# Kernel optimization log

Measured on AMD Instinct MI355X. Metric: run time of the kernel, lower is better.

## Reference

```python
import jax, jax.numpy as jnp
import numpy as np

THRESHOLD = 0.5
NEG_POS_RATIO = 3
ALPHA = 1.0
N_CLASSES = 81
B, P, M = 32, 8732, 16


def cxcy_to_xy(c):
    return jnp.concatenate([c[..., :2] - c[..., 2:] / 2, c[..., :2] + c[..., 2:] / 2], -1)


def xy_to_cxcy(x):
    return jnp.concatenate([(x[..., :2] + x[..., 2:]) / 2, x[..., 2:] - x[..., :2]], -1)


def cxcy_to_gcxgcy(c, p):
    # SSD box encoding with variances 0.1 / 0.2
    return jnp.concatenate([(c[..., :2] - p[..., :2]) / (p[..., 2:] / 10.0),
                            jnp.log(c[..., 2:] / p[..., 2:]) * 5.0], -1)


def box_iou(a, b):
    # a: [M,4], b: [P,4] in xy (xmin,ymin,xmax,ymax)
    lt = jnp.maximum(a[:, None, :2], b[None, :, :2])
    rb = jnp.minimum(a[:, None, 2:], b[None, :, 2:])
    wh = jnp.clip(rb - lt, 0.0)
    inter = wh[..., 0] * wh[..., 1]
    area_a = (a[:, 2] - a[:, 0]) * (a[:, 3] - a[:, 1])
    area_b = (b[:, 2] - b[:, 0]) * (b[:, 3] - b[:, 1])
    return inter / (area_a[:, None] + area_b[None, :] - inter)


def setup_inputs() -> dict:
    key = jax.random.key(0)
    k1, k2, k3, k4, k5, k6, k7 = jax.random.split(key, 7)
    predicted_locs = jax.random.normal(k1, (B, P, 4), dtype=jnp.float32)
    predicted_logits = jax.random.normal(k2, (B, P, N_CLASSES), dtype=jnp.float32)
    # valid gt boxes: centers in (0.2,0.8), sizes in (0.05,0.4) -> xy
    cxy = jax.random.uniform(k3, (B, M, 2), minval=0.2, maxval=0.8)
    wh = jax.random.uniform(k4, (B, M, 2), minval=0.05, maxval=0.4)
    boxes = cxcy_to_xy(jnp.concatenate([cxy, wh], -1)).astype(jnp.float32)
    labels = jax.random.randint(k5, (B, M), 1, N_CLASSES)  # real objects: labels >= 1
    # priors: centers in (0,1), positive sizes
    pcxy = jax.random.uniform(k6, (P, 2), minval=0.0, maxval=1.0)
    pwh = jax.random.uniform(k7, (P, 2), minval=0.05, maxval=0.6)
    priors_cxcy = jnp.concatenate([pcxy, pwh], -1).astype(jnp.float32)
    return {"predicted_locs": predicted_locs, "predicted_logits": predicted_logits,
            "boxes": boxes, "labels": labels, "priors_cxcy": priors_cxcy}


def reference(predicted_locs, predicted_logits, boxes, labels, priors_cxcy):
    priors_xy = cxcy_to_xy(priors_cxcy)

    def match(bx, lb):  # bx: [M,4] xy, lb: [M] int
        overlap = box_iou(bx, priors_xy)                # [M, P]
        overlap_for_each_prior = overlap.max(axis=0)    # [P]
        object_for_each_prior = overlap.argmax(axis=0)  # [P]
        prior_for_each_object = overlap.argmax(axis=1)  # [M]
        # force each gt object to be matched to its best prior
        object_for_each_prior = object_for_each_prior.at[prior_for_each_object].set(jnp.arange(M))
        overlap_for_each_prior = overlap_for_each_prior.at[prior_for_each_object].set(1.0)
        label_for_each_prior = lb[object_for_each_prior]
        label_for_each_prior = jnp.where(overlap_for_each_prior < THRESHOLD, 0, label_for_each_prior)
        true_locs = cxcy_to_gcxgcy(xy_to_cxcy(bx[object_for_each_prior]), priors_cxcy)
        return true_locs, label_for_each_prior

    true_locs, true_classes = jax.vmap(match)(boxes, labels)  # [B,P,4], [B,P]

    positive = true_classes != 0                 # [B,P]
    n_positives = positive.sum(axis=1)           # [B]
    n_pos_total = n_positives.sum().astype(jnp.float32)

    # localization: L1Loss (mean) over positive priors only -> mean over 4*n_pos elements
    loc_loss = jnp.sum(jnp.abs(predicted_locs - true_locs) * positive[..., None]) / (4.0 * n_pos_total)

    # per-prior cross entropy, nan/inf -> 0 as in the original
    logp = jax.nn.log_softmax(predicted_logits, axis=-1)
    conf_loss_all = -jnp.take_along_axis(logp, true_classes[..., None], axis=-1)[..., 0]  # [B,P]
    conf_loss_all = jnp.nan_to_num(conf_loss_all, nan=0.0, posinf=0.0, neginf=0.0)

    conf_loss_pos_sum = jnp.sum(conf_loss_all * positive)
    conf_loss_neg = jnp.where(positive, 0.0, conf_loss_all)
    conf_loss_neg = -jnp.sort(-conf_loss_neg, axis=1)  # descending sort per image
    ranks = jnp.arange(P)[None, :]
    hard_negatives = ranks < (NEG_POS_RATIO * n_positives)[:, None]
    conf_loss_hard_neg_sum = jnp.sum(conf_loss_neg * hard_negatives)

    conf_loss = (conf_loss_hard_neg_sum + conf_loss_pos_sum) / n_pos_total
    return conf_loss + ALPHA * loc_loss
```

## Files before the change

kernel.cpp:

```cpp
#include <hip/hip_runtime.h>
#include <math.h>

#define BB 32
#define PP 8732
#define MM 16
#define NC 81
#define THRESH 0.5f
#define NPR 3
#define CHUNKS 16
#define CHUNK ((PP + CHUNKS - 1) / CHUNKS)
#define SBLK 64

__global__ void __launch_bounds__(256) match_part_kernel(
    const float* __restrict__ boxes,
    const float* __restrict__ priors,
    float* __restrict__ ovl,
    int* __restrict__ obj,
    unsigned long long* __restrict__ keys_part,
    unsigned* __restrict__ done)
{
    const int b = blockIdx.x / CHUNKS;
    const int c = blockIdx.x % CHUNKS;
    const int tid = threadIdx.x;
    if (blockIdx.x == 0 && tid == 0) *done = 0u;

    __shared__ float s_box[MM][4];
    __shared__ float s_area[MM];
    __shared__ float s_bv[4 * MM];
    __shared__ int   s_bi[4 * MM];

    if (tid < MM * 4) ((float*)s_box)[tid] = boxes[b * MM * 4 + tid];
    __syncthreads();
    if (tid < MM)
        s_area[tid] = (s_box[tid][2] - s_box[tid][0]) * (s_box[tid][3] - s_box[tid][1]);
    __syncthreads();

    float bestv[MM];
    int   bestp[MM];
#pragma unroll
    for (int m = 0; m < MM; ++m) { bestv[m] = -1.0f; bestp[m] = 0; }

    const int p0 = c * CHUNK;
    const int p1 = (p0 + CHUNK < PP) ? (p0 + CHUNK) : PP;
    for (int p = p0 + tid; p < p1; p += 256) {
        const float4 pr = ((const float4*)priors)[p];
        float px0 = pr.x - pr.z * 0.5f, py0 = pr.y - pr.w * 0.5f;
        float px1 = pr.x + pr.z * 0.5f, py1 = pr.y + pr.w * 0.5f;
        float parea = (px1 - px0) * (py1 - py0);
        float bv = -1.0f; int bm = 0;
#pragma unroll
        for (int m = 0; m < MM; ++m) {
            float lx = fmaxf(s_box[m][0], px0);
            float ly = fmaxf(s_box[m][1], py0);
            float rx = fminf(s_box[m][2], px1);
            float ry = fminf(s_box[m][3], py1);
            float w = fmaxf(rx - lx, 0.0f);
            float h = fmaxf(ry - ly, 0.0f);
            float inter = w * h;
            float iou = inter / (s_area[m] + parea - inter);
            if (iou > bv) { bv = iou; bm = m; }
            if (iou > bestv[m]) { bestv[m] = iou; bestp[m] = p; }
        }
        ovl[b * PP + p] = bv;
        obj[b * PP + p] = bm;
    }

    const int lane = tid & 63, wid = tid >> 6;
#pragma unroll
    for (int m = 0; m < MM; ++m) {
        float v = bestv[m]; int i = bestp[m];
        for (int off = 32; off > 0; off >>= 1) {
            float ov = __shfl_xor(v, off);
            int   oi = __shfl_xor(i, off);
            if (ov > v || (ov == v && oi < i)) { v = ov; i = oi; }
        }
        if (lane == 0) { s_bv[wid * MM + m] = v; s_bi[wid * MM + m] = i; }
    }
    __syncthreads();

    if (tid == 0) {
        for (int m = 0; m < MM; ++m) {
            float v = s_bv[m]; int i = s_bi[m];
            for (int w = 1; w < 4; ++w) {
                float ov = s_bv[w * MM + m]; int oi = s_bi[w * MM + m];
                if (ov > v || (ov == v && oi < i)) { v = ov; i = oi; }
            }
            if (v < 0.0f) v = 0.0f;
            keys_part[(b * CHUNKS + c) * MM + m] =
                ((unsigned long long)__float_as_uint(v) << 32) |
                (unsigned long long)(0x7FFFFFFFu - (unsigned)i);
        }
    }
}

__global__ void __launch_bounds__(256) conf_kernel(
    const float* __restrict__ logits,
    const float* __restrict__ plocs,
    const float* __restrict__ boxes,
    const int*   __restrict__ labels,
    const float* __restrict__ priors,
    const float* __restrict__ ovl,
    const int*   __restrict__ obj,
    const unsigned long long* __restrict__ keys_part,
    float* __restrict__ neg,
    int*   __restrict__ cnt_part,
    float* __restrict__ conf_part,
    float* __restrict__ loc_part)
{
    const int tid = threadIdx.x;
    const int lane = tid & 63;
    const int g = lane >> 4;
    const int i = lane & 15;
    const int b = blockIdx.x / SBLK;
    const int s = blockIdx.x % SBLK;

    __shared__ float s_box[MM][4];
    __shared__ int   s_lab[MM];
    __shared__ int   s_fp[MM];
    __shared__ unsigned long long s_keys[CHUNKS * MM];

    if (tid < MM * 4) ((float*)s_box)[tid] = boxes[b * MM * 4 + tid];
    if (tid < MM) s_lab[tid] = labels[b * MM + tid];
    s_keys[tid] = keys_part[b * CHUNKS * MM + tid];
    __syncthreads();
    if (tid < MM) {
        unsigned long long best = 0ull;
#pragma unroll
        for (int c = 0; c < CHUNKS; ++c) {
            unsigned long long k = s_keys[c * MM + tid];
            if (k > best) best = k;
        }
        s_fp[tid] = (int)(0x7FFFFFFFu - (unsigned)(best & 0xFFFFFFFFull));
    }
    __syncthreads();

    const int myfp = s_fp[i];

    const int w0 = s * 4 + (tid >> 6);
    const int GPI = PP / 4;

    int   pcnt = 0;
    float pconf = 0.0f, ploc = 0.0f;

    for (int wi = w0; wi < GPI; wi += SBLK * 4) {
        const int rp = wi * 4 + g;
        const int r = b * PP + rp;
        const float ov = ovl[r];
        const int om = obj[r];

        unsigned long long bal = __ballot(myfp == rp);
        unsigned gm = (unsigned)((bal >> (g * 16)) & 0xFFFFull);
        int o, cls;
        if (gm) { o = 31 - __clz(gm); cls = s_lab[o]; }
        else    { o = om; cls = (ov < THRESH) ? 0 : s_lab[om]; }

        const size_t base = (size_t)r * NC;
        float e0 = logits[base + i];
        float e1 = logits[base + 16 + i];
        float e2 = logits[base + 32 + i];
        float e3 = logits[base + 48 + i];
        float e4 = logits[base + 64 + i];
        float e5 = (i == 0) ? logits[base + 80] : -INFINITY;

        float mx = fmaxf(fmaxf(fmaxf(e0, e1), fmaxf(e2, e3)), fmaxf(e4, e5));
#pragma unroll
        for (int off = 8; off > 0; off >>= 1) mx = fmaxf(mx, __shfl_xor(mx, off));
        float sum = __expf(e0 - mx) + __expf(e1 - mx) + __expf(e2 - mx) +
                    __expf(e3 - mx) + __expf(e4 - mx) +
                    ((i == 0) ? __expf(e5 - mx) : 0.0f);
#pragma unroll
        for (int off = 8; off > 0; off >>= 1) sum += __shfl_xor(sum, off);

        const int k = cls >> 4, ci = cls & 15;
        float ek = (k == 0) ? e0 : (k == 1) ? e1 : (k == 2) ? e2 :
                   (k == 3) ? e3 : (k == 4) ? e4 : e5;
        float xc = __shfl(ek, (g << 4) + ci);
        float conf = mx + __logf(sum) - xc;
        if (!isfinite(conf)) conf = 0.0f;

        if (i == 0) {
            neg[r] = (cls == 0) ? conf : 0.0f;
            if (cls != 0) {
                pcnt += 1;
                pconf += conf;
                const float4 pr = ((const float4*)priors)[rp];
                float cx = (s_box[o][0] + s_box[o][2]) * 0.5f;
                float cy = (s_box[o][1] + s_box[o][3]) * 0.5f;
                float w4 = s_box[o][2] - s_box[o][0];
                float h4 = s_box[o][3] - s_box[o][1];
                float g0 = (cx - pr.x) / (pr.z / 10.0f);
                float g1 = (cy - pr.y) / (pr.w / 10.0f);
                float g2 = logf(w4 / pr.z) * 5.0f;
                float g3 = logf(h4 / pr.w) * 5.0f;
                const float4 pl = ((const float4*)plocs)[r];
                ploc += fabsf(pl.x - g0) + fabsf(pl.y - g1) +
                        fabsf(pl.z - g2) + fabsf(pl.w - g3);
            }
        }
    }

    __shared__ int   s4i[4];
    __shared__ float s4c[4], s4l[4];
#pragma unroll
    for (int off = 32; off > 0; off >>= 1) {
        pcnt  += __shfl_xor(pcnt, off);
        pconf += __shfl_xor(pconf, off);
        ploc  += __shfl_xor(ploc, off);
    }
    const int wv = tid >> 6;
    if (lane == 0) { s4i[wv] = pcnt; s4c[wv] = pconf; s4l[wv] = ploc; }
    __syncthreads();
    if (tid == 0) {
        cnt_part[blockIdx.x]  = s4i[0] + s4i[1] + s4i[2] + s4i[3];
        conf_part[blockIdx.x] = s4c[0] + s4c[1] + s4c[2] + s4c[3];
        loc_part[blockIdx.x]  = s4l[0] + s4l[1] + s4l[2] + s4l[3];
    }
}

#define TPK 1024
#define VPT ((PP + TPK - 1) / TPK)

__global__ void __launch_bounds__(TPK) topk_final_kernel(
    const float* __restrict__ neg, const int* __restrict__ cnt_part,
    const float* __restrict__ conf_part, const float* __restrict__ loc_part,
    float* __restrict__ hardneg, unsigned* __restrict__ done,
    float* __restrict__ out)
{
    const int b = blockIdx.x;
    const int tid = threadIdx.x;
    const int lane = tid & 63, wid = tid >> 6;
    __shared__ int s16a[16], s16b[16];
    __shared__ float s16f[16];
    __shared__ int s_k;
    __shared__ int s_last;

    if (tid < 64) {
        int c = cnt_part[b * SBLK + tid];
#pragma unroll
        for (int off = 32; off > 0; off >>= 1) c += __shfl_xor(c, off);
        if (tid == 0) s_k = NPR * c;
    }

    unsigned v[VPT];
#pragma unroll
    for (int j = 0; j < VPT; ++j) {
        int p = tid + j * TPK;
        v[j] = (p < PP) ? __float_as_uint(neg[b * PP + p]) : 0u;
    }
    __syncthreads();

    int K = s_k;
    if (K > PP) K = PP;
    if (K > 0) {
        unsigned lo = 0u;
        {
            const unsigned m1 = 0x40000000u;
            int c1 = 0;
#pragma unroll
            for (int j = 0; j < VPT; ++j) c1 += (v[j] >= m1);
#pragma unroll
            for (int off = 32; off > 0; off >>= 1) c1 += __shfl_xor(c1, off);
            if (lane == 0) s16a[wid] = c1;
            __syncthreads();
            int n1 = 0;
#pragma unroll
            for (int j = 0; j < 16; ++j) n1 += s16a[j];
            __syncthreads();
            if (n1 >= K) lo = m1;
        }
        unsigned span = 0x40000000u;
        for (int it = 0; it < 15; ++it) {
            span >>= 2;
            const unsigned m1 = lo + span;
            const unsigned m2 = lo + 2 * span;
            const unsigned m3 = lo + 3 * span;
            int c12 = 0, c3 = 0;
#pragma unroll
            for (int j = 0; j < VPT; ++j) {
                c12 += (v[j] >= m1) + ((int)(v[j] >= m2) << 16);
                c3  += (v[j] >= m3);
            }
#pragma unroll
            for (int off = 32; off > 0; off >>= 1) {
                c12 += __shfl_xor(c12, off);
                c3  += __shfl_xor(c3, off);
            }
            if (lane == 0) { s16a[wid] = c12; s16b[wid] = c3; }
            __syncthreads();
            int t12 = 0, t3 = 0;
#pragma unroll
            for (int j = 0; j < 16; ++j) { t12 += s16a[j]; t3 += s16b[j]; }
            __syncthreads();
            const int n1 = t12 & 0xFFFF, n2 = t12 >> 16, n3 = t3;
            lo = (n3 >= K) ? m3 : (n2 >= K) ? m2 : (n1 >= K) ? m1 : lo;
        }
        const unsigned kth = lo;

        int cgt = 0; float sgt = 0.0f;
#pragma unroll
        for (int j = 0; j < VPT; ++j) {
            if (v[j] > kth) { cgt++; sgt += __uint_as_float(v[j]); }
        }
#pragma unroll
        for (int off = 32; off > 0; off >>= 1) {
            cgt += __shfl_xor(cgt, off);
            sgt += __shfl_xor(sgt, off);
        }
        if (lane == 0) { s16a[wid] = cgt; s16f[wid] = sgt; }
        __syncthreads();
        if (tid == 0) {
            int cgt_t = 0; float sum_gt = 0.0f;
#pragma unroll
            for (int j = 0; j < 16; ++j) { cgt_t += s16a[j]; sum_gt += s16f[j]; }
            hardneg[b] = sum_gt + (float)(K - cgt_t) * __uint_as_float(kth);
        }
    } else {
        if (tid == 0) hardneg[b] = 0.0f;
    }

    __threadfence();
    if (tid == 0) {
        unsigned old = atomicAdd(done, 1u);
        s_last = (old == BB - 1) ? 1 : 0;
    }
    __syncthreads();
    if (!s_last) return;
    __threadfence();

    int np = 0; float cf = 0.0f, lc = 0.0f, hn = 0.0f;
    for (int j = tid; j < BB * SBLK; j += TPK) {
        np += cnt_part[j];
        cf += conf_part[j];
        lc += loc_part[j];
    }
    if (tid < BB) hn = hardneg[tid];
#pragma unroll
    for (int off = 32; off > 0; off >>= 1) {
        np += __shfl_xor(np, off);
        cf += __shfl_xor(cf, off);
        lc += __shfl_xor(lc, off);
        hn += __shfl_xor(hn, off);
    }
    __shared__ float s16l[16], s16h[16];
    if (lane == 0) { s16a[wid] = np; s16f[wid] = cf; s16l[wid] = lc; s16h[wid] = hn; }
    __syncthreads();
    if (tid == 0) {
        int npt_i = 0; float cft = 0.0f, lct = 0.0f, hnt = 0.0f;
#pragma unroll
        for (int j = 0; j < 16; ++j) {
            npt_i += s16a[j]; cft += s16f[j]; lct += s16l[j]; hnt += s16h[j];
        }
        float npt = (float)npt_i;
        out[0] = (hnt + cft) / npt + lct / (4.0f * npt);
    }
}

extern "C" void kernel_launch(void* const* d_in, const int* in_sizes, int n_in,
                              void* d_out, int out_size, void* d_ws, size_t ws_size,
                              hipStream_t stream) {
    (void)in_sizes; (void)n_in; (void)out_size; (void)ws_size;
    const float* plocs  = (const float*)d_in[0];
    const float* logits = (const float*)d_in[1];
    const float* boxes  = (const float*)d_in[2];
    const int*   labels = (const int*)d_in[3];
    const float* priors = (const float*)d_in[4];
    float* out = (float*)d_out;

    char* ws = (char*)d_ws;
    float* ovl      = (float*)ws; ws += (size_t)BB * PP * 4;
    int*   obj      = (int*)ws;   ws += (size_t)BB * PP * 4;
    float* neg      = (float*)ws; ws += (size_t)BB * PP * 4;
    unsigned long long* keys_part = (unsigned long long*)ws; ws += (size_t)BB * CHUNKS * MM * 8;
    int*   cnt_part  = (int*)ws;   ws += BB * SBLK * 4;
    float* conf_part = (float*)ws; ws += BB * SBLK * 4;
    float* loc_part  = (float*)ws; ws += BB * SBLK * 4;
    float* hardneg   = (float*)ws; ws += BB * 4;
    unsigned* done   = (unsigned*)ws; ws += 4;


    match_part_kernel<<<BB * CHUNKS, 256, 0, stream>>>(boxes, priors, ovl, obj,
                                                       keys_part, done);

    conf_kernel<<<BB * SBLK, 256, 0, stream>>>(logits, plocs, boxes, labels, priors,
                                               ovl, obj, keys_part, neg,
                                               cnt_part, conf_part, loc_part);

    topk_final_kernel<<<BB, TPK, 0, stream>>>(neg, cnt_part, conf_part, loc_part,
                                              hardneg, done, out);
}
```

Measured before the change: 81.15 us.

## Pack overlap and object index, move forced matching to a separate kernel

The match kernel now writes the per-prior best IoU and best object index as one 64-bit word instead of two separate arrays. A new single-block kernel reduces the per-chunk best-prior keys and overwrites the packed entries of the forced-match priors with IoU 1.0. This takes the ballot-based forced-match check and the per-block key reduction out of the conf kernel. The conf kernel also loads the first 64 logits per prior as one float4 per lane rather than four strided scalars, and picks the target logit by component and lane. In exchange there is an extra serialized launch, and the float4 loads are not 16-byte aligned because each row holds 81 floats.

```diff
diff --git a/kernel.cpp b/kernel.cpp
--- a/kernel.cpp
+++ b/kernel.cpp
@@ -14,8 +14,7 @@
 __global__ void __launch_bounds__(256) match_part_kernel(
     const float* __restrict__ boxes,
     const float* __restrict__ priors,
-    float* __restrict__ ovl,
-    int* __restrict__ obj,
+    unsigned long long* __restrict__ packed,
     unsigned long long* __restrict__ keys_part,
     unsigned* __restrict__ done)
 {
@@ -61,8 +60,9 @@
             if (iou > bv) { bv = iou; bm = m; }
             if (iou > bestv[m]) { bestv[m] = iou; bestp[m] = p; }
         }
-        ovl[b * PP + p] = bv;
-        obj[b * PP + p] = bm;
+        packed[b * PP + p] =
+            ((unsigned long long)__float_as_uint(bv < 0.0f ? 0.0f : bv) << 32) |
+            (unsigned long long)(unsigned)bm;
     }
 
     const int lane = tid & 63, wid = tid >> 6;
@@ -93,15 +93,39 @@
     }
 }
 
+__global__ void __launch_bounds__(512) force_match_kernel(
+    const unsigned long long* __restrict__ keys_part,
+    unsigned long long* __restrict__ packed)
+{
+    __shared__ int s_p[BB * MM];
+    const int tid = threadIdx.x;
+    const int b = tid >> 4, m = tid & 15;
+
+    unsigned long long best = 0ull;
+#pragma unroll
+    for (int c = 0; c < CHUNKS; ++c) {
+        unsigned long long k = keys_part[(b * CHUNKS + c) * MM + m];
+        if (k > best) best = k;
+    }
+    s_p[tid] = (int)(0x7FFFFFFFu - (unsigned)(best & 0xFFFFFFFFull));
+    __syncthreads();
+
+    if (m == 0) {
+        const unsigned long long one = (unsigned long long)__float_as_uint(1.0f) << 32;
+        for (int mm = 0; mm < MM; ++mm) {
+            int p = s_p[(b << 4) + mm];
+            packed[b * PP + p] = one | (unsigned long long)(unsigned)mm;
+        }
+    }
+}
+
 __global__ void __launch_bounds__(256) conf_kernel(
     const float* __restrict__ logits,
     const float* __restrict__ plocs,
     const float* __restrict__ boxes,
     const int*   __restrict__ labels,
     const float* __restrict__ priors,
-    const float* __restrict__ ovl,
-    const int*   __restrict__ obj,
-    const unsigned long long* __restrict__ keys_part,
+    const unsigned long long* __restrict__ packed,
     float* __restrict__ neg,
     int*   __restrict__ cnt_part,
     float* __restrict__ conf_part,
@@ -116,25 +140,10 @@
 
     __shared__ float s_box[MM][4];
     __shared__ int   s_lab[MM];
-    __shared__ int   s_fp[MM];
-    __shared__ unsigned long long s_keys[CHUNKS * MM];
 
     if (tid < MM * 4) ((float*)s_box)[tid] = boxes[b * MM * 4 + tid];
     if (tid < MM) s_lab[tid] = labels[b * MM + tid];
-    s_keys[tid] = keys_part[b * CHUNKS * MM + tid];
-    __syncthreads();
-    if (tid < MM) {
-        unsigned long long best = 0ull;
-#pragma unroll
-        for (int c = 0; c < CHUNKS; ++c) {
-            unsigned long long k = s_keys[c * MM + tid];
-            if (k > best) best = k;
-        }
-        s_fp[tid] = (int)(0x7FFFFFFFu - (unsigned)(best & 0xFFFFFFFFull));
-    }
-    __syncthreads();
-
-    const int myfp = s_fp[i];
+    __syncthreads();
 
     const int w0 = s * 4 + (tid >> 6);
     const int GPI = PP / 4;
@@ -145,36 +154,35 @@
     for (int wi = w0; wi < GPI; wi += SBLK * 4) {
         const int rp = wi * 4 + g;
         const int r = b * PP + rp;
-        const float ov = ovl[r];
-        const int om = obj[r];
-
-        unsigned long long bal = __ballot(myfp == rp);
-        unsigned gm = (unsigned)((bal >> (g * 16)) & 0xFFFFull);
-        int o, cls;
-        if (gm) { o = 31 - __clz(gm); cls = s_lab[o]; }
-        else    { o = om; cls = (ov < THRESH) ? 0 : s_lab[om]; }
+        const unsigned long long pk = packed[r];
+        const float ov = __uint_as_float((unsigned)(pk >> 32));
+        const int om = (int)(pk & 0xFFFFull);
+        const int cls = (ov < THRESH) ? 0 : s_lab[om];
 
         const size_t base = (size_t)r * NC;
-        float e0 = logits[base + i];
-        float e1 = logits[base + 16 + i];
-        float e2 = logits[base + 32 + i];
-        float e3 = logits[base + 48 + i];
+        const float4 f = *(const float4*)(logits + base + 4 * i);
         float e4 = logits[base + 64 + i];
         float e5 = (i == 0) ? logits[base + 80] : -INFINITY;
 
-        float mx = fmaxf(fmaxf(fmaxf(e0, e1), fmaxf(e2, e3)), fmaxf(e4, e5));
+        float mx = fmaxf(fmaxf(fmaxf(f.x, f.y), fmaxf(f.z, f.w)), fmaxf(e4, e5));
 #pragma unroll
         for (int off = 8; off > 0; off >>= 1) mx = fmaxf(mx, __shfl_xor(mx, off));
-        float sum = __expf(e0 - mx) + __expf(e1 - mx) + __expf(e2 - mx) +
-                    __expf(e3 - mx) + __expf(e4 - mx) +
+        float sum = __expf(f.x - mx) + __expf(f.y - mx) + __expf(f.z - mx) +
+                    __expf(f.w - mx) + __expf(e4 - mx) +
                     ((i == 0) ? __expf(e5 - mx) : 0.0f);
 #pragma unroll
         for (int off = 8; off > 0; off >>= 1) sum += __shfl_xor(sum, off);
 
-        const int k = cls >> 4, ci = cls & 15;
-        float ek = (k == 0) ? e0 : (k == 1) ? e1 : (k == 2) ? e2 :
-                   (k == 3) ? e3 : (k == 4) ? e4 : e5;
-        float xc = __shfl(ek, (g << 4) + ci);
+        float xc;
+        if (cls < 64) {
+            const int comp = cls & 3;
+            float cand = comp == 0 ? f.x : comp == 1 ? f.y : comp == 2 ? f.z : f.w;
+            xc = __shfl(cand, (g << 4) + (cls >> 2));
+        } else if (cls < 80) {
+            xc = __shfl(e4, (g << 4) + (cls - 64));
+        } else {
+            xc = __shfl(e5, (g << 4));
+        }
         float conf = mx + __logf(sum) - xc;
         if (!isfinite(conf)) conf = 0.0f;
 
@@ -183,6 +191,7 @@
             if (cls != 0) {
                 pcnt += 1;
                 pconf += conf;
+                const int o = om;
                 const float4 pr = ((const float4*)priors)[rp];
                 float cx = (s_box[o][0] + s_box[o][2]) * 0.5f;
                 float cy = (s_box[o][1] + s_box[o][3]) * 0.5f;
@@ -367,10 +376,9 @@
     float* out = (float*)d_out;
 
     char* ws = (char*)d_ws;
-    float* ovl      = (float*)ws; ws += (size_t)BB * PP * 4;
-    int*   obj      = (int*)ws;   ws += (size_t)BB * PP * 4;
-    float* neg      = (float*)ws; ws += (size_t)BB * PP * 4;
+    unsigned long long* packed    = (unsigned long long*)ws; ws += (size_t)BB * PP * 8;
     unsigned long long* keys_part = (unsigned long long*)ws; ws += (size_t)BB * CHUNKS * MM * 8;
+    float* neg       = (float*)ws; ws += (size_t)BB * PP * 4;
     int*   cnt_part  = (int*)ws;   ws += BB * SBLK * 4;
     float* conf_part = (float*)ws; ws += BB * SBLK * 4;
     float* loc_part  = (float*)ws; ws += BB * SBLK * 4;
@@ -378,11 +386,13 @@
     unsigned* done   = (unsigned*)ws; ws += 4;
 
 
-    match_part_kernel<<<BB * CHUNKS, 256, 0, stream>>>(boxes, priors, ovl, obj,
+    match_part_kernel<<<BB * CHUNKS, 256, 0, stream>>>(boxes, priors, packed,
                                                        keys_part, done);
 
+    force_match_kernel<<<1, 512, 0, stream>>>(keys_part, packed);
+
     conf_kernel<<<BB * SBLK, 256, 0, stream>>>(logits, plocs, boxes, labels, priors,
-                                               ovl, obj, keys_part, neg,
+                                               packed, neg,
                                                cnt_part, conf_part, loc_part);
 
     topk_final_kernel<<<BB, TPK, 0, stream>>>(neg, cnt_part, conf_part, loc_part,
```

Result: no change. 82.60 us (+1.8%).

## Apply forced prior matches in a separate tiny kernel instead of per-iteration ballot

Applied to the files above, without the earlier changes.

Moves the forced best-prior-per-object assignment out of the conf kernel into a new single-block kernel that writes obj and ovl=1.0 directly for each object's best prior. The conf kernel then drops its shared-memory key reduction, two barriers and per-iteration ballot, reading labels and boxes straight from global memory. This trades per-block setup and per-row ballot work for an extra kernel launch and a serialized dependency between stages.

```diff
diff --git a/kernel.cpp b/kernel.cpp
--- a/kernel.cpp
+++ b/kernel.cpp
@@ -93,6 +93,32 @@
     }
 }
 
+__global__ void __launch_bounds__(512) force_match_kernel(
+    const unsigned long long* __restrict__ keys_part,
+    float* __restrict__ ovl, int* __restrict__ obj)
+{
+    __shared__ int s_p[BB * MM];
+    const int tid = threadIdx.x;
+    const int b = tid >> 4, m = tid & 15;
+
+    unsigned long long best = 0ull;
+#pragma unroll
+    for (int c = 0; c < CHUNKS; ++c) {
+        unsigned long long k = keys_part[(b * CHUNKS + c) * MM + m];
+        if (k > best) best = k;
+    }
+    s_p[tid] = (int)(0x7FFFFFFFu - (unsigned)(best & 0xFFFFFFFFull));
+    __syncthreads();
+
+    if (m == 0) {
+        for (int mm = 0; mm < MM; ++mm) {
+            int p = s_p[(b << 4) + mm];
+            obj[b * PP + p] = mm;
+            ovl[b * PP + p] = 1.0f;
+        }
+    }
+}
+
 __global__ void __launch_bounds__(256) conf_kernel(
     const float* __restrict__ logits,
     const float* __restrict__ plocs,
@@ -101,7 +127,6 @@
     const float* __restrict__ priors,
     const float* __restrict__ ovl,
     const int*   __restrict__ obj,
-    const unsigned long long* __restrict__ keys_part,
     float* __restrict__ neg,
     int*   __restrict__ cnt_part,
     float* __restrict__ conf_part,
@@ -113,29 +138,6 @@
     const int i = lane & 15;
     const int b = blockIdx.x / SBLK;
     const int s = blockIdx.x % SBLK;
-
-    __shared__ float s_box[MM][4];
-    __shared__ int   s_lab[MM];
-    __shared__ int   s_fp[MM];
-    __shared__ unsigned long long s_keys[CHUNKS * MM];
-
-    if (tid < MM * 4) ((float*)s_box)[tid] = boxes[b * MM * 4 + tid];
-    if (tid < MM) s_lab[tid] = labels[b * MM + tid];
-    s_keys[tid] = keys_part[b * CHUNKS * MM + tid];
-    __syncthreads();
-    if (tid < MM) {
-        unsigned long long best = 0ull;
-#pragma unroll
-        for (int c = 0; c < CHUNKS; ++c) {
-            unsigned long long k = s_keys[c * MM + tid];
-            if (k > best) best = k;
-        }
-        s_fp[tid] = (int)(0x7FFFFFFFu - (unsigned)(best & 0xFFFFFFFFull));
-    }
-    __syncthreads();
-
-    const int myfp = s_fp[i];
-
     const int w0 = s * 4 + (tid >> 6);
     const int GPI = PP / 4;
 
@@ -146,13 +148,8 @@
         const int rp = wi * 4 + g;
         const int r = b * PP + rp;
         const float ov = ovl[r];
-        const int om = obj[r];
-
-        unsigned long long bal = __ballot(myfp == rp);
-        unsigned gm = (unsigned)((bal >> (g * 16)) & 0xFFFFull);
-        int o, cls;
-        if (gm) { o = 31 - __clz(gm); cls = s_lab[o]; }
-        else    { o = om; cls = (ov < THRESH) ? 0 : s_lab[om]; }
+        const int o = obj[r];
+        const int lab = labels[b * MM + o];
 
         const size_t base = (size_t)r * NC;
         float e0 = logits[base + i];
@@ -171,6 +168,7 @@
 #pragma unroll
         for (int off = 8; off > 0; off >>= 1) sum += __shfl_xor(sum, off);
 
+        const int cls = (ov < THRESH) ? 0 : lab;
         const int k = cls >> 4, ci = cls & 15;
         float ek = (k == 0) ? e0 : (k == 1) ? e1 : (k == 2) ? e2 :
                    (k == 3) ? e3 : (k == 4) ? e4 : e5;
@@ -183,11 +181,12 @@
             if (cls != 0) {
                 pcnt += 1;
                 pconf += conf;
+                const float4 bx = ((const float4*)boxes)[b * MM + o];
+                float cx = (bx.x + bx.z) * 0.5f;
+                float cy = (bx.y + bx.w) * 0.5f;
+                float w4 = bx.z - bx.x;
+                float h4 = bx.w - bx.y;
                 const float4 pr = ((const float4*)priors)[rp];
-                float cx = (s_box[o][0] + s_box[o][2]) * 0.5f;
-                float cy = (s_box[o][1] + s_box[o][3]) * 0.5f;
-                float w4 = s_box[o][2] - s_box[o][0];
-                float h4 = s_box[o][3] - s_box[o][1];
                 float g0 = (cx - pr.x) / (pr.z / 10.0f);
                 float g1 = (cy - pr.y) / (pr.w / 10.0f);
                 float g2 = logf(w4 / pr.z) * 5.0f;
@@ -381,8 +380,10 @@
     match_part_kernel<<<BB * CHUNKS, 256, 0, stream>>>(boxes, priors, ovl, obj,
                                                        keys_part, done);
 
+    force_match_kernel<<<1, 512, 0, stream>>>(keys_part, ovl, obj);
+
     conf_kernel<<<BB * SBLK, 256, 0, stream>>>(logits, plocs, boxes, labels, priors,
-                                               ovl, obj, keys_part, neg,
+                                               ovl, obj, neg,
                                                cnt_part, conf_part, loc_part);
 
     topk_final_kernel<<<BB, TPK, 0, stream>>>(neg, cnt_part, conf_part, loc_part,
```

Result: slower. 83.01 us (+2.3%).
